# Kernel optimization log

Hardware: AMD Instinct MI355X
Metric: run time of the kernel (lower is better)

Reference implementation:

```python
import jax, jax.numpy as jnp
import numpy as np
import math

N = 65536   # number of tree nodes
K = 4       # branching factor of the complete K-ary tree
D = 300     # input_size
H = 256     # hidden_size

def _levels(n, k):
    # complete k-ary tree: level l spans [start, start + k**l)
    levels, start, size = [], 0, 1
    while start < n:
        end = min(start + size, n)
        levels.append((start, end))
        start, size = end, size * k
    return levels

LEVELS = _levels(N, K)

def setup_inputs() -> dict:
    key = jax.random.key(0)
    ks = jax.random.split(key, 16)
    def U(k, shape, s):
        return jax.random.uniform(k, shape, jnp.float32, -s, s)
    s1 = 1.0 / math.sqrt(D + H)
    sfi = 1.0 / math.sqrt(D)
    sfh = 1.0 / math.sqrt(H)
    return {
        "inputs": jax.random.normal(ks[0], (N, D), jnp.float32),
        "ix_w": U(ks[1], (H, D), s1), "ix_b": U(ks[2], (H,), s1),
        "ih_w": U(ks[3], (H, H), s1), "ih_b": U(ks[4], (H,), s1),
        "ux_w": U(ks[5], (H, D), s1), "ux_b": U(ks[6], (H,), s1),
        "uh_w": U(ks[7], (H, H), s1), "uh_b": U(ks[8], (H,), s1),
        "fi_w": U(ks[9], (H, D), sfi), "fi_b": U(ks[10], (H,), sfi),
        "fh_w": U(ks[11], (H, H), sfh), "fh_b": U(ks[12], (H,), sfh),
    }

def reference(inputs, ix_w, ix_b, ih_w, ih_b, ux_w, ux_b, uh_w, uh_b,
              fi_w, fi_b, fh_w, fh_b):
    # Precompute all input projections once (batched over every node).
    ix = inputs @ ix_w.T + ix_b   # [N, H]
    ux = inputs @ ux_w.T + ux_b   # [N, H]
    fi = inputs @ fi_w.T + fi_b   # [N, H]
    h = jnp.zeros((N, H), inputs.dtype)
    c = jnp.zeros((N, H), inputs.dtype)
    # Bottom-up over tree levels (children before parents); level bounds static.
    for (s, e) in reversed(LEVELS):
        node = jnp.arange(s, e)                                   # [L]
        cidx = node[:, None] * K + 1 + jnp.arange(K)[None, :]     # [L, K]
        valid = cidx < N
        cidx = jnp.where(valid, cidx, 0)
        m = valid[..., None].astype(inputs.dtype)                 # [L, K, 1]
        hc = h[cidx] * m                                          # [L, K, H]
        cc = c[cidx] * m
        h_sum = hc.sum(axis=1)                                    # [L, H]
        # per-child forget gate: sigmoid(W_fi x + b_fi + W_fh h_k + b_fh)
        f = jax.nn.sigmoid(fi[s:e][:, None, :]
                           + jnp.einsum('lkh,gh->lkg', hc, fh_w) + fh_b)
        fc = (f * cc).sum(axis=1)                                 # masked via cc
        i = jax.nn.sigmoid(ix[s:e] + h_sum @ ih_w.T + ih_b)
        u = jnp.tanh(ux[s:e] + h_sum @ uh_w.T + uh_b)
        c_new = i * u + fc
        h_new = jnp.tanh(c_new)          # no output gate in this module
        h = h.at[s:e].set(h_new)
        c = c.at[s:e].set(c_new)
    # root node state (matches (next_h, [next_h, next_c]) at the root)
    return h[0], c[0]
```

## Files before the change

kernel.cpp:

```cpp
#include <hip/hip_runtime.h>
#include <hip/hip_bf16.h>


#define NTOT 65536
#define DD   300
#define KP   320
#define HH   256
#define LEAF_START 16384
#define LOG2E 1.4426950408889634f

typedef unsigned short u16;
typedef unsigned int   u32;
typedef __attribute__((ext_vector_type(8))) short bf16x8;
typedef __attribute__((ext_vector_type(4))) float f32x4;

union BF8 { bf16x8 v; u16 u[8]; };

#define OFF_HB    0ull
#define OFF_CB    33554944ull
#define OFF_PRE   67109888ull
#define OFF_WXB   92275712ull
#define OFF_WHB   92767232ull
#define OFF_XB    93160448ull
#define OFF_PIU   135103488ull
#define OFF_FC    146375680ull
#define OFF_HSB   157647872ull
#define OFF_BI    166102016ull
#define OFF_BU    166103040ull
#define OFF_BF    166104064ull

__device__ __forceinline__ float frcp(float x) { return __builtin_amdgcn_rcpf(x); }
__device__ __forceinline__ float fex2(float x) { return __builtin_amdgcn_exp2f(x); }
__device__ __forceinline__ float sigm(float x)  { return frcp(1.f + fex2(-LOG2E * x)); }
__device__ __forceinline__ float ftanh(float x) { return 1.f - 2.f * frcp(1.f + fex2(2.f * LOG2E * x)); }

__device__ __forceinline__ u16 f2bf(float f) {
    __hip_bfloat16 b = __float2bfloat16(f);
    u16 u; __builtin_memcpy(&u, &b, 2); return u;
}
__device__ __forceinline__ float bf2f(u16 b) {
    union { u32 u; float f; } v; v.u = ((u32)b) << 16;
    return v.f;
}
__device__ __forceinline__ int lidx(int r, int g) { return (r << 3) | (g ^ (r & 7)); }

__device__ __forceinline__ void gll16(const void* g, void* l) {
    __builtin_amdgcn_global_load_lds(
        (const __attribute__((address_space(1))) unsigned int*)g,
        (__attribute__((address_space(3))) unsigned int*)l, 16, 0, 0);
}

__global__ __launch_bounds__(256) void conv_all(
    const float* __restrict__ X,
    const float* __restrict__ ixw, const float* __restrict__ uxw,
    const float* __restrict__ fiw,
    const float* __restrict__ ihw, const float* __restrict__ uhw,
    const float* __restrict__ fhw,
    const float* __restrict__ ixb, const float* __restrict__ ihb,
    const float* __restrict__ uxb, const float* __restrict__ uhb,
    const float* __restrict__ fib, const float* __restrict__ fhb,
    u32* __restrict__ Xb2, u32* __restrict__ Wxb2, u32* __restrict__ Whb2,
    u16* __restrict__ hb, u16* __restrict__ cb,
    float* __restrict__ bI, float* __restrict__ bU, float* __restrict__ bF)
{
    const int b = blockIdx.x;
    const int t = threadIdx.x;
    if (b < 2048) {
        const size_t total = (size_t)NTOT * 160;
        for (size_t id = (size_t)b * 256 + t; id < total; id += (size_t)2048 * 256) {
            const int node = (int)(id / 160);
            const int k    = ((int)(id % 160)) * 2;
            const float f0 = (k < DD)     ? X[(size_t)node * DD + k]     : 0.f;
            const float f1 = (k + 1 < DD) ? X[(size_t)node * DD + k + 1] : 0.f;
            Xb2[id] = (u32)f2bf(f0) | ((u32)f2bf(f1) << 16);
        }
    } else if (b < 2528) {
        const int b2 = b - 2048;
        const int total = 768 * 160;
        for (int id = b2 * 256 + t; id < total; id += 480 * 256) {
            const int row = id / 160;
            const int k   = (id % 160) * 2;
            const float* src = (row < 256) ? (ixw + (size_t)row * DD)
                             : (row < 512) ? (uxw + (size_t)(row - 256) * DD)
                                           : (fiw + (size_t)(row - 512) * DD);
            const float f0 = (k < DD)     ? src[k]     : 0.f;
            const float f1 = (k + 1 < DD) ? src[k + 1] : 0.f;
            Wxb2[id] = (u32)f2bf(f0) | ((u32)f2bf(f1) << 16);
        }
    } else {
        const int b3 = b - 2528;
        if (b3 == 0) {
            hb[(size_t)NTOT * HH + t] = 0;
            cb[(size_t)NTOT * HH + t] = 0;
            bI[t] = ixb[t] + ihb[t];
            bU[t] = uxb[t] + uhb[t];
            bF[t] = fib[t] + fhb[t];
        }
        const int total = 768 * 128;
        for (int id = b3 * 256 + t; id < total; id += 384 * 256) {
            const int row = id / 128;
            const int k   = (id % 128) * 2;
            const float* src = (row < 256) ? (ihw + (size_t)row * HH)
                             : (row < 512) ? (uhw + (size_t)(row - 256) * HH)
                                           : (fhw + (size_t)(row - 512) * HH);
            Whb2[id] = (u32)f2bf(src[k]) | ((u32)f2bf(src[k + 1]) << 16);
        }
    }
}

__global__ __launch_bounds__(256) void lp_gemm(
    const u16* __restrict__ Xb, const u16* __restrict__ Wxb,
    const float* __restrict__ bI, const float* __restrict__ bU,
    u16* __restrict__ hb, u16* __restrict__ cb, u16* __restrict__ pre)
{
    __shared__ bf16x8 Ash[2048];
    __shared__ bf16x8 Bsh[2048];

    const int tid  = threadIdx.x;
    const int lane = tid & 63;
    const int w    = tid >> 6;
    const int wr   = w >> 1, wc = w & 1;
    const int m16  = lane & 15, q = lane >> 4;

    const bf16x8* __restrict__ Xv = (const bf16x8*)Xb;
    const bf16x8* __restrict__ Wv = (const bf16x8*)Wxb;

    if (blockIdx.x < 1536) {
        const int row0   = LEAF_START + (blockIdx.x >> 2) * 128;
        const int chbase = (blockIdx.x & 3) * 64;

        auto stage = [&](int kt, int buf) {
            const int base = buf << 10;
            #pragma unroll
            for (int i = 0; i < 4; ++i) {
                const int sI = w * 256 + i * 64 + lane;
                const int r = sI >> 3, gs = sI & 7;
                const int g = gs ^ (r & 7);
                gll16(Xv + (size_t)(row0 + r) * 40 + kt * 8 + g, &Ash[base + sI]);
            }
            #pragma unroll
            for (int i = 0; i < 4; ++i) {
                const int sI = w * 256 + i * 64 + lane;
                const int br = sI >> 3, gs = sI & 7;
                const int g = gs ^ (br & 7);
                const int srow = ((br >> 6) << 8) + chbase + (br & 63);
                gll16(Wv + (size_t)srow * 40 + kt * 8 + g, &Bsh[base + sI]);
            }
        };

        f32x4 accI[4][2], accU[4][2];
        #pragma unroll
        for (int mf = 0; mf < 4; ++mf)
            #pragma unroll
            for (int nf = 0; nf < 2; ++nf) { accI[mf][nf] = (f32x4)0.f; accU[mf][nf] = (f32x4)0.f; }

        stage(0, 0);
        __syncthreads();
        for (int kt = 0; kt < 5; ++kt) {
            const int cur = kt & 1;
            if (kt < 4) stage(kt + 1, cur ^ 1);
            const int base = cur << 10;
            #pragma unroll
            for (int ks = 0; ks < 2; ++ks) {
                const int kg = ks * 4 + q;
                bf16x8 a[4], bIv[2], bUv[2];
                #pragma unroll
                for (int mf = 0; mf < 4; ++mf)
                    a[mf] = Ash[base + lidx(wr * 64 + mf * 16 + m16, kg)];
                #pragma unroll
                for (int nf = 0; nf < 2; ++nf) {
                    bIv[nf] = Bsh[base + lidx(wc * 32 + nf * 16 + m16, kg)];
                    bUv[nf] = Bsh[base + lidx(64 + wc * 32 + nf * 16 + m16, kg)];
                }
                #pragma unroll
                for (int mf = 0; mf < 4; ++mf)
                    #pragma unroll
                    for (int nf = 0; nf < 2; ++nf) {
                        accI[mf][nf] = __builtin_amdgcn_mfma_f32_16x16x32_bf16(
                            a[mf], bIv[nf], accI[mf][nf], 0, 0, 0);
                        accU[mf][nf] = __builtin_amdgcn_mfma_f32_16x16x32_bf16(
                            a[mf], bUv[nf], accU[mf][nf], 0, 0, 0);
                    }
            }
            __syncthreads();
        }

        #pragma unroll
        for (int nf = 0; nf < 2; ++nf) {
            const int ch = chbase + wc * 32 + nf * 16 + m16;
            const float bi = bI[ch];
            const float bu = bU[ch];
            #pragma unroll
            for (int mf = 0; mf < 4; ++mf) {
                #pragma unroll
                for (int r4 = 0; r4 < 4; ++r4) {
                    const float cn = sigm(accI[mf][nf][r4] + bi) * ftanh(accU[mf][nf][r4] + bu);
                    const int node = row0 + wr * 64 + mf * 16 + q * 4 + r4;
                    const size_t off = (size_t)node * HH + ch;
                    cb[off] = f2bf(cn);
                    hb[off] = f2bf(ftanh(cn));
                }
            }
        }
    } else {
        const int pb   = blockIdx.x - 1536;
        const int row0 = (pb / 6) * 128;
        const int n0   = (pb % 6) * 128;

        auto stage = [&](int kt, int buf) {
            const int base = buf << 10;
            #pragma unroll
            for (int i = 0; i < 4; ++i) {
                const int sI = w * 256 + i * 64 + lane;
                const int r = sI >> 3, gs = sI & 7;
                const int g = gs ^ (r & 7);
                gll16(Xv + (size_t)(row0 + r) * 40 + kt * 8 + g, &Ash[base + sI]);
            }
            #pragma unroll
            for (int i = 0; i < 4; ++i) {
                const int sI = w * 256 + i * 64 + lane;
                const int br = sI >> 3, gs = sI & 7;
                const int g = gs ^ (br & 7);
                gll16(Wv + (size_t)(n0 + br) * 40 + kt * 8 + g, &Bsh[base + sI]);
            }
        };

        f32x4 acc[4][4];
        #pragma unroll
        for (int mf = 0; mf < 4; ++mf)
            #pragma unroll
            for (int nf = 0; nf < 4; ++nf) acc[mf][nf] = (f32x4)0.f;

        stage(0, 0);
        __syncthreads();
        for (int kt = 0; kt < 5; ++kt) {
            const int cur = kt & 1;
            if (kt < 4) stage(kt + 1, cur ^ 1);
            const int base = cur << 10;
            #pragma unroll
            for (int ks = 0; ks < 2; ++ks) {
                const int kg = ks * 4 + q;
                bf16x8 a[4], b[4];
                #pragma unroll
                for (int mf = 0; mf < 4; ++mf)
                    a[mf] = Ash[base + lidx(wr * 64 + mf * 16 + m16, kg)];
                #pragma unroll
                for (int nf = 0; nf < 4; ++nf)
                    b[nf] = Bsh[base + lidx(wc * 64 + nf * 16 + m16, kg)];
                #pragma unroll
                for (int mf = 0; mf < 4; ++mf)
                    #pragma unroll
                    for (int nf = 0; nf < 4; ++nf)
                        acc[mf][nf] = __builtin_amdgcn_mfma_f32_16x16x32_bf16(
                            a[mf], b[nf], acc[mf][nf], 0, 0, 0);
            }
            __syncthreads();
        }

        #pragma unroll
        for (int mf = 0; mf < 4; ++mf)
            #pragma unroll
            for (int nf = 0; nf < 4; ++nf) {
                const int col = n0 + wc * 64 + nf * 16 + m16;
                #pragma unroll
                for (int r4 = 0; r4 < 4; ++r4) {
                    const int node = row0 + wr * 64 + mf * 16 + q * 4 + r4;
                    pre[(size_t)node * 768 + col] = f2bf(acc[mf][nf][r4]);
                }
            }
    }
}

__global__ __launch_bounds__(256) void rec_gemm(
    const u16* __restrict__ hb, const u16* __restrict__ hsb,
    const u16* __restrict__ Whb, const u16* __restrict__ pre,
    const float* __restrict__ bF, const u16* __restrict__ cb,
    u16* __restrict__ projIU, float* __restrict__ fcbuf,
    int s, int crow0, int L, int bigIU)
{
    __shared__ bf16x8 Ash[2048];
    __shared__ bf16x8 Bsh[2048];

    const int nIUrb = (L + 127) >> 7;
    const int bid   = blockIdx.x;

    bool isIU; int rb, cbk;
    if (bid < nIUrb * 4) { isIU = true;  rb = bid >> 2; cbk = bid & 3; }
    else { isIU = false; const int b2 = bid - nIUrb * 4; rb = b2 >> 1; cbk = b2 & 1; }

    const int row0  = rb * 128;
    const int Brow0 = isIU ? cbk * 128 : 512 + cbk * 128;
    const int ocol0 = cbk * 128;

    const int tid  = threadIdx.x;
    const int lane = tid & 63;
    const int w    = tid >> 6;
    const int wr   = w >> 1, wc = w & 1;
    const int m16  = lane & 15, q = lane >> 4;

    const bf16x8* __restrict__ Hv = (const bf16x8*)hb;
    const bf16x8* __restrict__ Sv = (const bf16x8*)hsb;
    const bf16x8* __restrict__ Wv = (const bf16x8*)Whb;

    auto stage = [&](int kt, int buf) {
        const int base = buf << 10;
        if (isIU && bigIU) {
            #pragma unroll
            for (int i = 0; i < 4; ++i) {
                const int G = tid + i * 256;
                const int r = G >> 3, g = G & 7;
                bf16x8 val;
                if (row0 + r < L) {
                    const size_t cg0 = (size_t)(crow0 + 4 * (row0 + r)) * 32 + kt * 8 + g;
                    BF8 x0, x1, x2, x3, o;
                    x0.v = Hv[cg0]; x1.v = Hv[cg0 + 32];
                    x2.v = Hv[cg0 + 64]; x3.v = Hv[cg0 + 96];
                    #pragma unroll
                    for (int j = 0; j < 8; ++j)
                        o.u[j] = f2bf(bf2f(x0.u[j]) + bf2f(x1.u[j])
                                    + bf2f(x2.u[j]) + bf2f(x3.u[j]));
                    val = o.v;
                } else {
                    BF8 z;
                    #pragma unroll
                    for (int j = 0; j < 8; ++j) z.u[j] = 0;
                    val = z.v;
                }
                Ash[base + lidx(r, g)] = val;
            }
        } else {
            #pragma unroll
            for (int i = 0; i < 4; ++i) {
                const int sI = w * 256 + i * 64 + lane;
                const int r = sI >> 3, gs = sI & 7;
                const int g = gs ^ (r & 7);
                if (isIU) {
                    gll16(Sv + (size_t)(s + row0 + r) * 32 + kt * 8 + g, &Ash[base + sI]);
                } else {
                    int arow = crow0 + row0 + r;
                    if (arow > NTOT) arow = NTOT;
                    gll16(Hv + (size_t)arow * 32 + kt * 8 + g, &Ash[base + sI]);
                }
            }
        }
        #pragma unroll
        for (int i = 0; i < 4; ++i) {
            const int sI = w * 256 + i * 64 + lane;
            const int br = sI >> 3, gs = sI & 7;
            const int g = gs ^ (br & 7);
            gll16(Wv + (size_t)(Brow0 + br) * 32 + kt * 8 + g, &Bsh[base + sI]);
        }
    };

    f32x4 acc[4][4];
    #pragma unroll
    for (int mf = 0; mf < 4; ++mf)
        #pragma unroll
        for (int nf = 0; nf < 4; ++nf) acc[mf][nf] = (f32x4)0.f;

    stage(0, 0);
    __syncthreads();
    for (int kt = 0; kt < 4; ++kt) {
        const int cur = kt & 1;
        if (kt < 3) stage(kt + 1, cur ^ 1);
        const int base = cur << 10;
        #pragma unroll
        for (int ks = 0; ks < 2; ++ks) {
            const int kg = ks * 4 + q;
            bf16x8 a[4], b[4];
            #pragma unroll
            for (int mf = 0; mf < 4; ++mf)
                a[mf] = Ash[base + lidx(wr * 64 + mf * 16 + m16, kg)];
            #pragma unroll
            for (int nf = 0; nf < 4; ++nf)
                b[nf] = Bsh[base + lidx(wc * 64 + nf * 16 + m16, kg)];
            #pragma unroll
            for (int mf = 0; mf < 4; ++mf)
                #pragma unroll
                for (int nf = 0; nf < 4; ++nf)
                    acc[mf][nf] = __builtin_amdgcn_mfma_f32_16x16x32_bf16(
                        a[mf], b[nf], acc[mf][nf], 0, 0, 0);
        }
        __syncthreads();
    }

    if (isIU) {
        #pragma unroll
        for (int mf = 0; mf < 4; ++mf)
            #pragma unroll
            for (int nf = 0; nf < 4; ++nf) {
                const int col = ocol0 + wc * 64 + nf * 16 + m16;
                #pragma unroll
                for (int r4 = 0; r4 < 4; ++r4) {
                    const int orow = row0 + wr * 64 + mf * 16 + q * 4 + r4;
                    projIU[(size_t)orow * 512 + col] = f2bf(acc[mf][nf][r4]);
                }
            }
    } else {
        #pragma unroll
        for (int mf = 0; mf < 4; ++mf) {
            const int off  = wr * 64 + mf * 16 + q * 4;
            const int goff = (row0 + off) >> 2;
            if (goff < L) {
                #pragma unroll
                for (int nf = 0; nf < 4; ++nf) {
                    const int col = ocol0 + wc * 64 + nf * 16 + m16;
                    const float fpre = bf2f(pre[(size_t)(s + goff) * 768 + 512 + col]) + bF[col];
                    float fc = 0.f;
                    #pragma unroll
                    for (int r4 = 0; r4 < 4; ++r4) {
                        int child = crow0 + row0 + off + r4;
                        if (child > NTOT) child = NTOT;
                        const float cc = bf2f(cb[(size_t)child * HH + col]);
                        fc = fmaf(sigm(acc[mf][nf][r4] + fpre), cc, fc);
                    }
                    fcbuf[(size_t)goff * HH + col] = fc;
                }
            }
        }
    }
}

__global__ __launch_bounds__(256) void gate_kernel(
    const u32* __restrict__ pre2, const u32* __restrict__ pIU2,
    const float* __restrict__ fcbuf,
    const float* __restrict__ bI, const float* __restrict__ bU,
    u32* __restrict__ hb2, u32* __restrict__ cb2, u32* __restrict__ hsumb2,
    float* __restrict__ out, int s, int L)
{
    const int t  = threadIdx.x;
    const int j2 = t & 127;

    if (L == 1) {
        if (t >= 128) return;
        const float2 vbi = ((const float2*)bI)[j2];
        const float2 vbu = ((const float2*)bU)[j2];
        const u32 pi = pre2[j2];
        const u32 pu = pre2[128 + j2];
        const u32 ri = pIU2[j2];
        const u32 ru = pIU2[128 + j2];
        const float aI0 = bf2f((u16)pi) + bf2f((u16)ri) + vbi.x;
        const float aI1 = bf2f((u16)(pi >> 16)) + bf2f((u16)(ri >> 16)) + vbi.y;
        const float aU0 = bf2f((u16)pu) + bf2f((u16)ru) + vbu.x;
        const float aU1 = bf2f((u16)(pu >> 16)) + bf2f((u16)(ru >> 16)) + vbu.y;
        const float2 fc = ((const float2*)fcbuf)[j2];
        const float cn0 = fmaf(sigm(aI0), ftanh(aU0), fc.x);
        const float cn1 = fmaf(sigm(aI1), ftanh(aU1), fc.y);
        const float hn0 = ftanh(cn0);
        const float hn1 = ftanh(cn1);
        hb2[j2] = (u32)f2bf(hn0) | ((u32)f2bf(hn1) << 16);
        cb2[j2] = (u32)f2bf(cn0) | ((u32)f2bf(cn1) << 16);
        ((float2*)out)[j2] = make_float2(hn0, hn1);
        ((float2*)(out + 256))[j2] = make_float2(cn0, cn1);
        return;
    }

    const int ng = (L + 3) >> 2;
    const int gateBlocks = (ng + 1) >> 1;
    if ((int)blockIdx.x >= gateBlocks) {
        const int id = ((int)blockIdx.x - gateBlocks) * 256 + t;
        if (id < 1365 * 128) {
            const int ploc = id >> 7, jj = id & 127;
            const int p = 4096 + ploc;
            const int c0 = 4 * p + 1;
            float s0 = 0.f, s1 = 0.f;
            #pragma unroll
            for (int k = 0; k < 4; ++k) {
                const u32 v = hb2[(size_t)(c0 + k) * 128 + jj];
                s0 += bf2f((u16)v);
                s1 += bf2f((u16)(v >> 16));
            }
            hsumb2[(size_t)p * 128 + jj] = (u32)f2bf(s0) | ((u32)f2bf(s1) << 16);
        }
        return;
    }

    const float2 vbi = ((const float2*)bI)[j2];
    const float2 vbu = ((const float2*)bU)[j2];
    const int g = blockIdx.x * 2 + (t >> 7);
    if (g >= ng) return;
    const int p = ((s - 1) >> 2) + g;

    float hs0 = 0.f, hs1 = 0.f;
    #pragma unroll
    for (int k = 0; k < 4; ++k) {
        const int nloc = 4 * g + k;
        const int n = s + nloc;
        if (nloc < L) {
            const u32 pi = pre2[(size_t)n * 384 + j2];
            const u32 pu = pre2[(size_t)n * 384 + 128 + j2];
            const u32 ri = pIU2[(size_t)nloc * 256 + j2];
            const u32 ru = pIU2[(size_t)nloc * 256 + 128 + j2];
            const float aI0 = bf2f((u16)pi) + bf2f((u16)ri) + vbi.x;
            const float aI1 = bf2f((u16)(pi >> 16)) + bf2f((u16)(ri >> 16)) + vbi.y;
            const float aU0 = bf2f((u16)pu) + bf2f((u16)ru) + vbu.x;
            const float aU1 = bf2f((u16)(pu >> 16)) + bf2f((u16)(ru >> 16)) + vbu.y;
            const float2 fc = ((const float2*)fcbuf)[(size_t)nloc * 128 + j2];
            const float cn0 = fmaf(sigm(aI0), ftanh(aU0), fc.x);
            const float cn1 = fmaf(sigm(aI1), ftanh(aU1), fc.y);
            const float hn0 = ftanh(cn0);
            const float hn1 = ftanh(cn1);
            hb2[(size_t)n * 128 + j2] = (u32)f2bf(hn0) | ((u32)f2bf(hn1) << 16);
            cb2[(size_t)n * 128 + j2] = (u32)f2bf(cn0) | ((u32)f2bf(cn1) << 16);
            hs0 += hn0; hs1 += hn1;
        } else {
            const u32 v = hb2[(size_t)n * 128 + j2];
            hs0 += bf2f((u16)v);
            hs1 += bf2f((u16)(v >> 16));
        }
    }
    hsumb2[(size_t)p * 128 + j2] = (u32)f2bf(hs0) | ((u32)f2bf(hs1) << 16);
}

extern "C" void kernel_launch(void* const* d_in, const int* in_sizes, int n_in,
                              void* d_out, int out_size, void* d_ws, size_t ws_size,
                              hipStream_t stream) {
    const float* X   = (const float*)d_in[0];
    const float* ixw = (const float*)d_in[1];
    const float* ixb = (const float*)d_in[2];
    const float* ihw = (const float*)d_in[3];
    const float* ihb = (const float*)d_in[4];
    const float* uxw = (const float*)d_in[5];
    const float* uxb = (const float*)d_in[6];
    const float* uhw = (const float*)d_in[7];
    const float* uhb = (const float*)d_in[8];
    const float* fiw = (const float*)d_in[9];
    const float* fib = (const float*)d_in[10];
    const float* fhw = (const float*)d_in[11];
    const float* fhb = (const float*)d_in[12];
    float* out = (float*)d_out;

    char* ws = (char*)d_ws;
    u16* hb   = (u16*)(ws + OFF_HB);
    u16* cb   = (u16*)(ws + OFF_CB);
    u16* pre  = (u16*)(ws + OFF_PRE);
    u16* Wxb  = (u16*)(ws + OFF_WXB);
    u16* Whb  = (u16*)(ws + OFF_WHB);
    u16* Xb   = (u16*)(ws + OFF_XB);
    u16* pIU  = (u16*)(ws + OFF_PIU);
    float* fc = (float*)(ws + OFF_FC);
    u16* hsb  = (u16*)(ws + OFF_HSB);
    float* bI = (float*)(ws + OFF_BI);
    float* bU = (float*)(ws + OFF_BU);
    float* bF = (float*)(ws + OFF_BF);

    conv_all<<<2912, 256, 0, stream>>>(X, ixw, uxw, fiw, ihw, uhw, fhw,
        ixb, ihb, uxb, uhb, fib, fhb,
        (u32*)Xb, (u32*)Wxb, (u32*)Whb, hb, cb, bI, bU, bF);

    lp_gemm<<<2304, 256, 0, stream>>>(Xb, Wxb, bI, bU, hb, cb, pre);

    const int starts[8] = {5461, 1365, 341, 85, 21, 5, 1, 0};
    const int ends[8]   = {16384, 5461, 1365, 341, 85, 21, 5, 1};
    for (int l = 0; l < 8; ++l) {
        const int s = starts[l], e = ends[l];
        const int L = e - s;
        const int crow0 = 4 * s + 1;
        const int nIUrb = (L + 127) >> 7;
        const int nFrb  = (4 * L + 127) >> 7;
        rec_gemm<<<nIUrb * 4 + nFrb * 2, 256, 0, stream>>>(hb, hsb, Whb, pre, bF, cb,
            pIU, fc, s, crow0, L, (l == 0) ? 1 : 0);
        const int ng = (L + 3) >> 2;
        const int gateBlocks = (ng + 1) >> 1;
        const int hsBlocks = (l == 0) ? 683 : 0;
        gate_kernel<<<gateBlocks + hsBlocks, 256, 0, stream>>>(
            (const u32*)pre, (const u32*)pIU, fc, bI, bU,
            (u32*)hb, (u32*)cb, (u32*)hsb, out, s, L);
    }
}
```

Before: 198.3 us.

## Fuse upper tree levels into one persistent kernel with grid barriers

Replaces the per-level rec_gemm and gate_kernel launches for the seven upper tree levels with a single persistent 256-block kernel. That kernel loops over levels and separates phases with an atomic-counter grid barrier. The intent is to remove the launch overhead and idle gaps of the many small dependent launches near the root. The cost is spin-wait barrier overhead, and the kernel relies on all 256 blocks being co-resident; if they are not, it deadlocks.

```diff
diff --git a/kernel.cpp b/kernel.cpp
--- a/kernel.cpp
+++ b/kernel.cpp
@@ -8,6 +8,7 @@
 #define HH   256
 #define LEAF_START 16384
 #define LOG2E 1.4426950408889634f
+#define TGRID 256
 
 typedef unsigned short u16;
 typedef unsigned int   u32;
@@ -28,6 +29,7 @@
 #define OFF_BI    166102016ull
 #define OFF_BU    166103040ull
 #define OFF_BF    166104064ull
+#define OFF_CTR   166105088ull
 
 __device__ __forceinline__ float frcp(float x) { return __builtin_amdgcn_rcpf(x); }
 __device__ __forceinline__ float fex2(float x) { return __builtin_amdgcn_exp2f(x); }
@@ -48,6 +50,18 @@
     __builtin_amdgcn_global_load_lds(
         (const __attribute__((address_space(1))) unsigned int*)g,
         (__attribute__((address_space(3))) unsigned int*)l, 16, 0, 0);
+}
+
+__device__ __forceinline__ void gridbar(u32* ctr, int gen) {
+    __syncthreads();
+    if (threadIdx.x == 0) {
+        __hip_atomic_fetch_add(ctr, 1u, __ATOMIC_RELEASE, __HIP_MEMORY_SCOPE_AGENT);
+        while (__hip_atomic_load(ctr, __ATOMIC_ACQUIRE, __HIP_MEMORY_SCOPE_AGENT)
+               < (u32)(TGRID * gen)) {
+            __builtin_amdgcn_s_sleep(8);
+        }
+    }
+    __syncthreads();
 }
 
 __global__ __launch_bounds__(256) void conv_all(
@@ -271,22 +285,19 @@
     }
 }
 
-__global__ __launch_bounds__(256) void rec_gemm(
+__device__ __forceinline__ void rec_tile_body(
+    bf16x8* __restrict__ Ash, bf16x8* __restrict__ Bsh,
     const u16* __restrict__ hb, const u16* __restrict__ hsb,
     const u16* __restrict__ Whb, const u16* __restrict__ pre,
     const float* __restrict__ bF, const u16* __restrict__ cb,
     u16* __restrict__ projIU, float* __restrict__ fcbuf,
-    int s, int crow0, int L, int bigIU)
+    int s, int crow0, int L, int bigIU, int tileId)
 {
-    __shared__ bf16x8 Ash[2048];
-    __shared__ bf16x8 Bsh[2048];
-
     const int nIUrb = (L + 127) >> 7;
-    const int bid   = blockIdx.x;
 
     bool isIU; int rb, cbk;
-    if (bid < nIUrb * 4) { isIU = true;  rb = bid >> 2; cbk = bid & 3; }
-    else { isIU = false; const int b2 = bid - nIUrb * 4; rb = b2 >> 1; cbk = b2 & 1; }
+    if (tileId < nIUrb * 4) { isIU = true;  rb = tileId >> 2; cbk = tileId & 3; }
+    else { isIU = false; const int b2 = tileId - nIUrb * 4; rb = b2 >> 1; cbk = b2 & 1; }
 
     const int row0  = rb * 128;
     const int Brow0 = isIU ? cbk * 128 : 512 + cbk * 128;
@@ -421,7 +432,8 @@
     }
 }
 
-__global__ __launch_bounds__(256) void gate_kernel(
+__device__ __forceinline__ void gate_chunk_body(
+    int c,
     const u32* __restrict__ pre2, const u32* __restrict__ pIU2,
     const float* __restrict__ fcbuf,
     const float* __restrict__ bI, const float* __restrict__ bU,
@@ -432,7 +444,7 @@
     const int j2 = t & 127;
 
     if (L == 1) {
-        if (t >= 128) return;
+        if (c != 0 || t >= 128) return;
         const float2 vbi = ((const float2*)bI)[j2];
         const float2 vbu = ((const float2*)bU)[j2];
         const u32 pi = pre2[j2];
@@ -456,28 +468,9 @@
     }
 
     const int ng = (L + 3) >> 2;
-    const int gateBlocks = (ng + 1) >> 1;
-    if ((int)blockIdx.x >= gateBlocks) {
-        const int id = ((int)blockIdx.x - gateBlocks) * 256 + t;
-        if (id < 1365 * 128) {
-            const int ploc = id >> 7, jj = id & 127;
-            const int p = 4096 + ploc;
-            const int c0 = 4 * p + 1;
-            float s0 = 0.f, s1 = 0.f;
-            #pragma unroll
-            for (int k = 0; k < 4; ++k) {
-                const u32 v = hb2[(size_t)(c0 + k) * 128 + jj];
-                s0 += bf2f((u16)v);
-                s1 += bf2f((u16)(v >> 16));
-            }
-            hsumb2[(size_t)p * 128 + jj] = (u32)f2bf(s0) | ((u32)f2bf(s1) << 16);
-        }
-        return;
-    }
-
     const float2 vbi = ((const float2*)bI)[j2];
     const float2 vbu = ((const float2*)bU)[j2];
-    const int g = blockIdx.x * 2 + (t >> 7);
+    const int g = c * 2 + (t >> 7);
     if (g >= ng) return;
     const int p = ((s - 1) >> 2) + g;
 
@@ -512,6 +505,82 @@
     hsumb2[(size_t)p * 128 + j2] = (u32)f2bf(hs0) | ((u32)f2bf(hs1) << 16);
 }
 
+__global__ __launch_bounds__(256) void rec_gemm0(
+    const u16* __restrict__ hb, const u16* __restrict__ hsb,
+    const u16* __restrict__ Whb, const u16* __restrict__ pre,
+    const float* __restrict__ bF, const u16* __restrict__ cb,
+    u16* __restrict__ projIU, float* __restrict__ fcbuf,
+    int s, int crow0, int L)
+{
+    __shared__ bf16x8 Ash[2048];
+    __shared__ bf16x8 Bsh[2048];
+    rec_tile_body(Ash, Bsh, hb, hsb, Whb, pre, bF, cb, projIU, fcbuf,
+                  s, crow0, L, 1, blockIdx.x);
+}
+
+__global__ __launch_bounds__(256) void gate0_kernel(
+    const u32* __restrict__ pre2, const u32* __restrict__ pIU2,
+    const float* __restrict__ fcbuf,
+    const float* __restrict__ bI, const float* __restrict__ bU,
+    u32* __restrict__ hb2, u32* __restrict__ cb2, u32* __restrict__ hsumb2,
+    float* __restrict__ out, int s, int L, int gateBlocks)
+{
+    const int t = threadIdx.x;
+    if ((int)blockIdx.x >= gateBlocks) {
+        const int id = ((int)blockIdx.x - gateBlocks) * 256 + t;
+        if (id < 1365 * 128) {
+            const int ploc = id >> 7, jj = id & 127;
+            const int p = 4096 + ploc;
+            const int c0 = 4 * p + 1;
+            float s0 = 0.f, s1 = 0.f;
+            #pragma unroll
+            for (int k = 0; k < 4; ++k) {
+                const u32 v = hb2[(size_t)(c0 + k) * 128 + jj];
+                s0 += bf2f((u16)v);
+                s1 += bf2f((u16)(v >> 16));
+            }
+            hsumb2[(size_t)p * 128 + jj] = (u32)f2bf(s0) | ((u32)f2bf(s1) << 16);
+        }
+        return;
+    }
+    gate_chunk_body(blockIdx.x, pre2, pIU2, fcbuf, bI, bU,
+                    hb2, cb2, hsumb2, out, s, L);
+}
+
+__global__ __launch_bounds__(256) void tail_kernel(
+    const u16* __restrict__ hb, const u16* __restrict__ hsb,
+    const u16* __restrict__ Whb, const u16* __restrict__ pre,
+    const float* __restrict__ bF, const u16* __restrict__ cb,
+    u16* __restrict__ projIU, float* __restrict__ fcbuf,
+    const float* __restrict__ bI, const float* __restrict__ bU,
+    float* __restrict__ out, u32* __restrict__ ctr)
+{
+    __shared__ bf16x8 Ash[2048];
+    __shared__ bf16x8 Bsh[2048];
+
+    const int starts[7] = {1365, 341, 85, 21, 5, 1, 0};
+    const int Ls[7]     = {4096, 1024, 256, 64, 16, 4, 1};
+
+    int gen = 0;
+    for (int l = 0; l < 7; ++l) {
+        const int s = starts[l], L = Ls[l];
+        const int crow0 = 4 * s + 1;
+        const int nIUrb = (L + 127) >> 7;
+        const int nFrb  = (4 * L + 127) >> 7;
+        const int Trec  = nIUrb * 4 + nFrb * 2;
+        for (int tIdx = blockIdx.x; tIdx < Trec; tIdx += TGRID)
+            rec_tile_body(Ash, Bsh, hb, hsb, Whb, pre, bF, cb, projIU, fcbuf,
+                          s, crow0, L, 0, tIdx);
+        gridbar(ctr, ++gen);
+        const int ng = (L + 3) >> 2;
+        const int CH = (L == 1) ? 1 : ((ng + 1) >> 1);
+        for (int c = blockIdx.x; c < CH; c += TGRID)
+            gate_chunk_body(c, (const u32*)pre, (const u32*)projIU, fcbuf, bI, bU,
+                            (u32*)hb, (u32*)cb, (u32*)hsb, out, s, L);
+        if (l < 6) gridbar(ctr, ++gen);
+    }
+}
+
 extern "C" void kernel_launch(void* const* d_in, const int* in_sizes, int n_in,
                               void* d_out, int out_size, void* d_ws, size_t ws_size,
                               hipStream_t stream) {
@@ -543,6 +612,9 @@
     float* bI = (float*)(ws + OFF_BI);
     float* bU = (float*)(ws + OFF_BU);
     float* bF = (float*)(ws + OFF_BF);
+    u32* ctr  = (u32*)(ws + OFF_CTR);
+
+    hipMemsetAsync(ctr, 0, 4, stream);
 
     conv_all<<<2912, 256, 0, stream>>>(X, ixw, uxw, fiw, ihw, uhw, fhw,
         ixb, ihb, uxb, uhb, fib, fhb,
@@ -550,21 +622,19 @@
 
     lp_gemm<<<2304, 256, 0, stream>>>(Xb, Wxb, bI, bU, hb, cb, pre);
 
-    const int starts[8] = {5461, 1365, 341, 85, 21, 5, 1, 0};
-    const int ends[8]   = {16384, 5461, 1365, 341, 85, 21, 5, 1};
-    for (int l = 0; l < 8; ++l) {
-        const int s = starts[l], e = ends[l];
-        const int L = e - s;
-        const int crow0 = 4 * s + 1;
+    {
+        const int s = 5461, L = 10923, crow0 = 21845;
         const int nIUrb = (L + 127) >> 7;
         const int nFrb  = (4 * L + 127) >> 7;
-        rec_gemm<<<nIUrb * 4 + nFrb * 2, 256, 0, stream>>>(hb, hsb, Whb, pre, bF, cb,
-            pIU, fc, s, crow0, L, (l == 0) ? 1 : 0);
+        rec_gemm0<<<nIUrb * 4 + nFrb * 2, 256, 0, stream>>>(
+            hb, hsb, Whb, pre, bF, cb, pIU, fc, s, crow0, L);
         const int ng = (L + 3) >> 2;
         const int gateBlocks = (ng + 1) >> 1;
-        const int hsBlocks = (l == 0) ? 683 : 0;
-        gate_kernel<<<gateBlocks + hsBlocks, 256, 0, stream>>>(
+        gate0_kernel<<<gateBlocks + 683, 256, 0, stream>>>(
             (const u32*)pre, (const u32*)pIU, fc, bI, bU,
-            (u32*)hb, (u32*)cb, (u32*)hsb, out, s, L);
-    }
-}
+            (u32*)hb, (u32*)cb, (u32*)hsb, out, s, L, gateBlocks);
+    }
+
+    tail_kernel<<<TGRID, 256, 0, stream>>>(hb, hsb, Whb, pre, bF, cb,
+                                           pIU, fc, bI, bU, out, ctr);
+}
```

Measured after the change: 400.6 us. 2.02x slower.

## Load weight fragments directly from global memory and widen leaf-block tiles

Applied to the files above, without the earlier changes.

The input-projection GEMM stops staging weight tiles through shared memory. Each wave now reads its B fragments straight from global memory (relying on L1/L2 cache reuse), which halves LDS use and removes the B staging loads. Leaf blocks also cover 128 channels instead of 64, so the grid drops from 2304 to 1536 blocks and the X tile is reused across more outputs. The cost is uncoalesced, per-lane global loads sitting inside the MFMA inner loop, where they may stall. Leaf blocks also hold twice as many accumulator registers, which can lower occupancy.

```diff
diff --git a/kernel.cpp b/kernel.cpp
--- a/kernel.cpp
+++ b/kernel.cpp
@@ -114,7 +114,6 @@
     u16* __restrict__ hb, u16* __restrict__ cb, u16* __restrict__ pre)
 {
     __shared__ bf16x8 Ash[2048];
-    __shared__ bf16x8 Bsh[2048];
 
     const int tid  = threadIdx.x;
     const int lane = tid & 63;
@@ -125,69 +124,63 @@
     const bf16x8* __restrict__ Xv = (const bf16x8*)Xb;
     const bf16x8* __restrict__ Wv = (const bf16x8*)Wxb;
 
-    if (blockIdx.x < 1536) {
-        const int row0   = LEAF_START + (blockIdx.x >> 2) * 128;
-        const int chbase = (blockIdx.x & 3) * 64;
-
-        auto stage = [&](int kt, int buf) {
-            const int base = buf << 10;
-            #pragma unroll
-            for (int i = 0; i < 4; ++i) {
-                const int sI = w * 256 + i * 64 + lane;
-                const int r = sI >> 3, gs = sI & 7;
-                const int g = gs ^ (r & 7);
-                gll16(Xv + (size_t)(row0 + r) * 40 + kt * 8 + g, &Ash[base + sI]);
-            }
-            #pragma unroll
-            for (int i = 0; i < 4; ++i) {
-                const int sI = w * 256 + i * 64 + lane;
-                const int br = sI >> 3, gs = sI & 7;
-                const int g = gs ^ (br & 7);
-                const int srow = ((br >> 6) << 8) + chbase + (br & 63);
-                gll16(Wv + (size_t)srow * 40 + kt * 8 + g, &Bsh[base + sI]);
-            }
-        };
-
-        f32x4 accI[4][2], accU[4][2];
+    const bool isLeaf = blockIdx.x < 768;
+    const int row0 = isLeaf ? (LEAF_START + (blockIdx.x >> 1) * 128)
+                            : ((blockIdx.x - 768) / 6 * 128);
+    const int cb0  = isLeaf ? ((blockIdx.x & 1) * 128)
+                            : ((blockIdx.x - 768) % 6 * 128);
+
+    auto stageA = [&](int kt, int buf) {
+        const int base = buf << 10;
+        #pragma unroll
+        for (int i = 0; i < 4; ++i) {
+            const int sI = w * 256 + i * 64 + lane;
+            const int r = sI >> 3, gs = sI & 7;
+            const int g = gs ^ (r & 7);
+            gll16(Xv + (size_t)(row0 + r) * 40 + kt * 8 + g, &Ash[base + sI]);
+        }
+    };
+
+    if (isLeaf) {
+        f32x4 accI[4][4], accU[4][4];
         #pragma unroll
         for (int mf = 0; mf < 4; ++mf)
             #pragma unroll
-            for (int nf = 0; nf < 2; ++nf) { accI[mf][nf] = (f32x4)0.f; accU[mf][nf] = (f32x4)0.f; }
-
-        stage(0, 0);
+            for (int nf = 0; nf < 4; ++nf) { accI[mf][nf] = (f32x4)0.f; accU[mf][nf] = (f32x4)0.f; }
+
+        stageA(0, 0);
         __syncthreads();
         for (int kt = 0; kt < 5; ++kt) {
             const int cur = kt & 1;
-            if (kt < 4) stage(kt + 1, cur ^ 1);
+            if (kt < 4) stageA(kt + 1, cur ^ 1);
             const int base = cur << 10;
             #pragma unroll
             for (int ks = 0; ks < 2; ++ks) {
                 const int kg = ks * 4 + q;
-                bf16x8 a[4], bIv[2], bUv[2];
+                bf16x8 a[4];
                 #pragma unroll
                 for (int mf = 0; mf < 4; ++mf)
                     a[mf] = Ash[base + lidx(wr * 64 + mf * 16 + m16, kg)];
                 #pragma unroll
-                for (int nf = 0; nf < 2; ++nf) {
-                    bIv[nf] = Bsh[base + lidx(wc * 32 + nf * 16 + m16, kg)];
-                    bUv[nf] = Bsh[base + lidx(64 + wc * 32 + nf * 16 + m16, kg)];
-                }
-                #pragma unroll
-                for (int mf = 0; mf < 4; ++mf)
+                for (int nf = 0; nf < 4; ++nf) {
+                    const int chrow = cb0 + wc * 64 + nf * 16 + m16;
+                    const bf16x8 bIv = Wv[(size_t)chrow * 40 + kt * 8 + kg];
+                    const bf16x8 bUv = Wv[(size_t)(256 + chrow) * 40 + kt * 8 + kg];
                     #pragma unroll
-                    for (int nf = 0; nf < 2; ++nf) {
+                    for (int mf = 0; mf < 4; ++mf) {
                         accI[mf][nf] = __builtin_amdgcn_mfma_f32_16x16x32_bf16(
-                            a[mf], bIv[nf], accI[mf][nf], 0, 0, 0);
+                            a[mf], bIv, accI[mf][nf], 0, 0, 0);
                         accU[mf][nf] = __builtin_amdgcn_mfma_f32_16x16x32_bf16(
-                            a[mf], bUv[nf], accU[mf][nf], 0, 0, 0);
+                            a[mf], bUv, accU[mf][nf], 0, 0, 0);
                     }
+                }
             }
             __syncthreads();
         }
 
         #pragma unroll
-        for (int nf = 0; nf < 2; ++nf) {
-            const int ch = chbase + wc * 32 + nf * 16 + m16;
+        for (int nf = 0; nf < 4; ++nf) {
+            const int ch = cb0 + wc * 64 + nf * 16 + m16;
             const float bi = bI[ch];
             const float bu = bU[ch];
             #pragma unroll
@@ -203,56 +196,34 @@
             }
         }
     } else {
-        const int pb   = blockIdx.x - 1536;
-        const int row0 = (pb / 6) * 128;
-        const int n0   = (pb % 6) * 128;
-
-        auto stage = [&](int kt, int buf) {
-            const int base = buf << 10;
-            #pragma unroll
-            for (int i = 0; i < 4; ++i) {
-                const int sI = w * 256 + i * 64 + lane;
-                const int r = sI >> 3, gs = sI & 7;
-                const int g = gs ^ (r & 7);
-                gll16(Xv + (size_t)(row0 + r) * 40 + kt * 8 + g, &Ash[base + sI]);
-            }
-            #pragma unroll
-            for (int i = 0; i < 4; ++i) {
-                const int sI = w * 256 + i * 64 + lane;
-                const int br = sI >> 3, gs = sI & 7;
-                const int g = gs ^ (br & 7);
-                gll16(Wv + (size_t)(n0 + br) * 40 + kt * 8 + g, &Bsh[base + sI]);
-            }
-        };
-
         f32x4 acc[4][4];
         #pragma unroll
         for (int mf = 0; mf < 4; ++mf)
             #pragma unroll
             for (int nf = 0; nf < 4; ++nf) acc[mf][nf] = (f32x4)0.f;
 
-        stage(0, 0);
+        stageA(0, 0);
         __syncthreads();
         for (int kt = 0; kt < 5; ++kt) {
             const int cur = kt & 1;
-            if (kt < 4) stage(kt + 1, cur ^ 1);
+            if (kt < 4) stageA(kt + 1, cur ^ 1);
             const int base = cur << 10;
             #pragma unroll
             for (int ks = 0; ks < 2; ++ks) {
                 const int kg = ks * 4 + q;
-                bf16x8 a[4], b[4];
+                bf16x8 a[4];
                 #pragma unroll
                 for (int mf = 0; mf < 4; ++mf)
                     a[mf] = Ash[base + lidx(wr * 64 + mf * 16 + m16, kg)];
                 #pragma unroll
-                for (int nf = 0; nf < 4; ++nf)
-                    b[nf] = Bsh[base + lidx(wc * 64 + nf * 16 + m16, kg)];
-                #pragma unroll
-                for (int mf = 0; mf < 4; ++mf)
+                for (int nf = 0; nf < 4; ++nf) {
+                    const int wrow = cb0 + wc * 64 + nf * 16 + m16;
+                    const bf16x8 bv = Wv[(size_t)wrow * 40 + kt * 8 + kg];
                     #pragma unroll
-                    for (int nf = 0; nf < 4; ++nf)
+                    for (int mf = 0; mf < 4; ++mf)
                         acc[mf][nf] = __builtin_amdgcn_mfma_f32_16x16x32_bf16(
-                            a[mf], b[nf], acc[mf][nf], 0, 0, 0);
+                            a[mf], bv, acc[mf][nf], 0, 0, 0);
+                }
             }
             __syncthreads();
         }
@@ -261,7 +232,7 @@
         for (int mf = 0; mf < 4; ++mf)
             #pragma unroll
             for (int nf = 0; nf < 4; ++nf) {
-                const int col = n0 + wc * 64 + nf * 16 + m16;
+                const int col = cb0 + wc * 64 + nf * 16 + m16;
                 #pragma unroll
                 for (int r4 = 0; r4 < 4; ++r4) {
                     const int node = row0 + wr * 64 + mf * 16 + q * 4 + r4;
@@ -548,7 +519,7 @@
         ixb, ihb, uxb, uhb, fib, fhb,
         (u32*)Xb, (u32*)Wxb, (u32*)Whb, hb, cb, bI, bU, bF);
 
-    lp_gemm<<<2304, 256, 0, stream>>>(Xb, Wxb, bI, bU, hb, cb, pre);
+    lp_gemm<<<1536, 256, 0, stream>>>(Xb, Wxb, bI, bU, hb, cb, pre);
 
     const int starts[8] = {5461, 1365, 341, 85, 21, 5, 1, 0};
     const int ends[8]   = {16384, 5461, 1365, 341, 85, 21, 5, 1};
```

Result: slower. 235.7 us (+18.9%).
